# Kernel optimization log

Measured on AMD Instinct MI355X. Metric: run time of the kernel, lower is better.

The kernel has to match this reference:

```python
import jax, jax.numpy as jnp
import numpy as np

B, N, K, D, H = 4, 256, 32, 32, 8
NUM_SPATIAL, NUM_EDGES = 512, 1024


def setup_inputs() -> dict:
    key = jax.random.key(0)
    k1, k2, k3, k4, k5 = jax.random.split(key, 5)
    spatial_pos = jax.random.randint(k1, (B, N, N), 0, NUM_SPATIAL, dtype=jnp.int64)
    edge_input = jax.random.randint(k2, (B, N, N, K), 0, NUM_EDGES + 1, dtype=jnp.int64)
    spatial_emb = jax.random.normal(k3, (NUM_SPATIAL, H), dtype=jnp.float32)
    spatial_emb = spatial_emb.at[0].set(0.0)  # padding_idx=0
    edge_feat_emb = jax.random.normal(k4, (NUM_EDGES + 1, D), dtype=jnp.float32)
    edge_feat_emb = edge_feat_emb.at[0].set(0.0)  # padding_idx=0
    edge_pos_emb = jax.random.normal(k5, (K, D * H), dtype=jnp.float32)
    return {"spatial_pos": spatial_pos, "edge_input": edge_input,
            "spatial_emb": spatial_emb, "edge_feat_emb": edge_feat_emb,
            "edge_pos_emb": edge_pos_emb}


def reference(spatial_pos, edge_input, spatial_emb, edge_feat_emb, edge_pos_emb):
    # spatial bias: gather [B,N,N,H] -> [B,H,N,N]
    spatial_bias = jnp.transpose(spatial_emb[spatial_pos], (0, 3, 1, 2))
    # edge feature gather: [B,N,N,K,D]
    edge_feat = edge_feat_emb[edge_input]
    pos_weight = edge_pos_emb.reshape(K, D, H)  # [K,D,H]
    # per-hop projection then mean over valid hops
    terms = jnp.einsum('bnmkd,kdh->bnmkh', edge_feat, pos_weight)  # [B,N,N,K,H]
    mask = (edge_input != 0)
    path_len = jnp.maximum(mask.sum(axis=-1, keepdims=True).astype(terms.dtype), 1.0)  # [B,N,N,1]
    edge_bias = terms.sum(axis=-2) / path_len  # [B,N,N,H]
    edge_bias = jnp.transpose(edge_bias, (0, 3, 1, 2))  # [B,H,N,N]
    return spatial_bias + edge_bias
```

## Files before the change

kernel.cpp:

```cpp
#include <hip/hip_runtime.h>
#include <hip/hip_bf16.h>

#define BB 4
#define NN 256
#define KK 32
#define DD 32
#define HH 8
#define NROWS 1024
#define NPTS (BB * NN * NN)
#define NNSQ (NN * NN)
#define TPB 1024
#define NBLK (NPTS / TPB)
#define SLICE_US (NROWS * HH)
#define SLOT_US  (2 * SLICE_US)

typedef __attribute__((ext_vector_type(8))) unsigned short ushort8;
typedef __attribute__((ext_vector_type(4))) int iv4;

#define FENCE  asm volatile("" ::: "memory")
#define LGKM0  asm volatile("s_waitcnt lgkmcnt(0)" ::: "memory")
#define BAR    __builtin_amdgcn_s_barrier()
#define VMW(n) asm volatile("s_waitcnt vmcnt(" #n ")" ::: "memory")

__device__ __forceinline__ unsigned short f2bf(float f) {
    unsigned u = __float_as_uint(f);
    unsigned r = (u + 0x7FFFu + ((u >> 16) & 1u)) >> 16;
    return (unsigned short)r;
}

__device__ __forceinline__ void gload16(const void* g, void* l) {
    __builtin_amdgcn_global_load_lds(
        (const __attribute__((address_space(1))) void*)g,
        (__attribute__((address_space(3))) void*)l,
        16, 0, 0);
}

__global__ __launch_bounds__(256) void build_proj_bf16(
    const float* __restrict__ feat,
    const float* __restrict__ w,
    unsigned short* __restrict__ proj)
{
    int t  = blockIdx.x * 256 + threadIdx.x;
    int k  = t >> 10;
    int e  = (t & 1023) + 1;

    const float* frow = feat + (size_t)e * DD;
    const float* wrow = w + (size_t)k * DD * HH;

    float acc[HH];
#pragma unroll
    for (int h = 0; h < HH; ++h) acc[h] = 0.0f;

#pragma unroll
    for (int d = 0; d < DD; ++d) {
        float f = frow[d];
#pragma unroll
        for (int h = 0; h < HH; ++h) acc[h] = fmaf(f, wrow[d * HH + h], acc[h]);
    }

    ushort8 o;
#pragma unroll
    for (int h = 0; h < HH; ++h) o[h] = f2bf(acc[h]);
    *(ushort8*)(proj + (size_t)t * HH) = o;
}

template <int E>
__global__ __launch_bounds__(TPB) void attn_bias_v8(
    const int* __restrict__ sp,
    const int* __restrict__ ei,
    const float* __restrict__ semb,
    const unsigned short* __restrict__ proj,
    float* __restrict__ out)
{
    __shared__ __align__(16) unsigned short tbuf[3 * SLOT_US];
    __shared__ __align__(16) unsigned short zrow[8];
    __shared__ unsigned int ibuf[2][4][NROWS + 4];

    const int tid = threadIdx.x;
    const int p0  = blockIdx.x * TPB;
    const int pg  = p0 + tid;

    constexpr int NC = (E == 2) ? 4 : 2;
    const iv4* EI4 = (const iv4*)ei;
    const size_t bi4 = (size_t)p0 * (8 * E);

    iv4 cv[NC];

    auto issueC = [&](int g) {
#pragma unroll
        for (int c = 0; c < NC; ++c) {
            if (E == 2) {
                int j = c * TPB + tid, pt = j >> 2, q = j & 3;
                cv[c] = EI4[bi4 + (size_t)pt * 16 + 4 * g + q];
            } else {
                int j = c * TPB + tid, pt = j >> 1, q = j & 1;
                cv[c] = EI4[bi4 + (size_t)pt * 8 + 2 * g + q];
            }
        }
    };
    auto writeC = [&](int nb) {
#pragma unroll
        for (int c = 0; c < NC; ++c) {
            if (E == 2) {
                int j = c * TPB + tid, pt = j >> 2, q = j & 3;
                ibuf[nb][q][pt] = ((unsigned)cv[c].x & 0xffffu) |
                                  ((unsigned)cv[c].z << 16);
            } else {
                int j = c * TPB + tid, pt = j >> 1, q = j & 1;
                ibuf[nb][2 * q][pt] = ((unsigned)cv[c].x & 0xffffu) |
                                      ((unsigned)cv[c].y << 16);
                ibuf[nb][2 * q + 1][pt] = ((unsigned)cv[c].z & 0xffffu) |
                                          ((unsigned)cv[c].w << 16);
            }
        }
    };
    auto stage2 = [&](int phn, int slot) {
        gload16(proj + (size_t)(2 * phn) * SLICE_US + tid * HH,
                &tbuf[slot * SLOT_US + tid * HH]);
        gload16(proj + (size_t)(2 * phn + 1) * SLICE_US + tid * HH,
                &tbuf[slot * SLOT_US + SLICE_US + tid * HH]);
    };

    float acc[HH];
#pragma unroll
    for (int h = 0; h < HH; ++h) acc[h] = 0.0f;
    int cnt = 0;

    auto dohops = [&](int slot, int gsel, int q) {
        unsigned pr = ibuf[gsel][q][tid];
        int e0 = pr & 0xffffu;
        int e1 = pr >> 16;
        cnt += (e0 != 0) + (e1 != 0);
        const unsigned short* tb = &tbuf[slot * SLOT_US];
        const unsigned short* a0 = e0 ? tb + (e0 - 1) * HH : zrow;
        const unsigned short* a1 = e1 ? tb + SLICE_US + (e1 - 1) * HH : zrow;
        ushort8 w0 = *(const ushort8*)a0;
        ushort8 w1 = *(const ushort8*)a1;
#pragma unroll
        for (int h = 0; h < HH; ++h) {
            acc[h] += __uint_as_float(((unsigned)w0[h]) << 16);
            acc[h] += __uint_as_float(((unsigned)w1[h]) << 16);
        }
    };

#define VMWA do { if constexpr (E == 2) VMW(6); else VMW(4); } while (0)
#define ENDPH do { FENCE; VMW(2); LGKM0; BAR; } while (0)

    int sv = (E == 2) ? (int)((const long long*)sp)[pg] : sp[pg];
    FENCE;
    issueC(0);
    FENCE;
    stage2(0, 0);
    stage2(1, 1);
    if (tid == 0) *(float4*)zrow = make_float4(0.f, 0.f, 0.f, 0.f);
    FENCE;
    writeC(0);
    issueC(1);
    FENCE;
    VMWA; LGKM0; BAR;

    stage2(2, 2);  FENCE; dohops(0, 0, 0); FENCE; VMWA; LGKM0; BAR;
    stage2(3, 0);  FENCE; dohops(1, 0, 1); ENDPH;
    stage2(4, 1);  FENCE; dohops(2, 0, 2); ENDPH;
    stage2(5, 2);  FENCE; dohops(0, 0, 3); writeC(1); issueC(2);
                   FENCE; VMWA; LGKM0; BAR;
    stage2(6, 0);  FENCE; dohops(1, 1, 0); FENCE; VMWA; LGKM0; BAR;
    stage2(7, 1);  FENCE; dohops(2, 1, 1); ENDPH;
    stage2(8, 2);  FENCE; dohops(0, 1, 2); ENDPH;
    stage2(9, 0);  FENCE; dohops(1, 1, 3); writeC(0); issueC(3);
                   FENCE; VMWA; LGKM0; BAR;
    stage2(10, 1); FENCE; dohops(2, 0, 0); FENCE; VMWA; LGKM0; BAR;
    stage2(11, 2); FENCE; dohops(0, 0, 1); ENDPH;
    stage2(12, 0); FENCE; dohops(1, 0, 2); ENDPH;
    stage2(13, 1); FENCE; dohops(2, 0, 3); writeC(1); ENDPH;
    stage2(14, 2); FENCE; dohops(0, 1, 0); ENDPH;
    stage2(15, 0); FENCE; dohops(1, 1, 1); ENDPH;
    dohops(2, 1, 2); FENCE; VMW(0); LGKM0; BAR;
    dohops(0, 1, 3);

    const float4* srow = (const float4*)(semb + (size_t)sv * HH);
    float4 s0v = srow[0], s1v = srow[1];
    float sb[HH] = {s0v.x, s0v.y, s0v.z, s0v.w, s1v.x, s1v.y, s1v.z, s1v.w};

    float inv = 1.0f / (float)(cnt ? cnt : 1);
    float* o = out + (size_t)(pg >> 16) * (HH * NNSQ) + (pg & (NNSQ - 1));
#pragma unroll
    for (int h = 0; h < HH; ++h)
        o[(size_t)h * NNSQ] = sb[h] + acc[h] * inv;
}

extern "C" void kernel_launch(void* const* d_in, const int* in_sizes, int n_in,
                              void* d_out, int out_size, void* d_ws, size_t ws_size,
                              hipStream_t stream) {
    const int*   sp = (const int*)d_in[0];
    const int*   ei = (const int*)d_in[1];
    const float* se = (const float*)d_in[2];
    const float* fe = (const float*)d_in[3];
    const float* pw = (const float*)d_in[4];
    float* out = (float*)d_out;

    const bool i64 = (in_sizes[0] == 2 * NPTS);
    unsigned short* proj = (unsigned short*)d_ws;

    build_proj_bf16<<<128, 256, 0, stream>>>(fe, pw, proj);

    if (i64) attn_bias_v8<2><<<NBLK, TPB, 0, stream>>>(sp, ei, se, proj, out);
    else     attn_bias_v8<1><<<NBLK, TPB, 0, stream>>>(sp, ei, se, proj, out);
}
```

Measured before the change: 25.81 us.

## Precompact edge indices to 16-bit pairs in a fused pre-pass kernel

```diff
diff --git a/kernel.cpp b/kernel.cpp
--- a/kernel.cpp
+++ b/kernel.cpp
@@ -13,9 +13,14 @@
 #define NBLK (NPTS / TPB)
 #define SLICE_US (NROWS * HH)
 #define SLOT_US  (2 * SLICE_US)
+#define CMP_U32 (NPTS * 16)
+#define CMP_BYTES ((size_t)CMP_U32 * 4)
+#define PROJ_BYTES ((size_t)KK * NROWS * HH * 2)
+#define NEED_WS (CMP_BYTES + PROJ_BYTES)
 
 typedef __attribute__((ext_vector_type(8))) unsigned short ushort8;
 typedef __attribute__((ext_vector_type(4))) int iv4;
+typedef __attribute__((ext_vector_type(2))) int iv2;
 
 #define FENCE  asm volatile("" ::: "memory")
 #define LGKM0  asm volatile("s_waitcnt lgkmcnt(0)" ::: "memory")
@@ -35,45 +40,151 @@
         16, 0, 0);
 }
 
+__device__ __forceinline__ void build_one(int t, const float* __restrict__ feat,
+                                          const float* __restrict__ w,
+                                          unsigned short* __restrict__ proj) {
+    int k = t >> 10;
+    int e = (t & 1023) + 1;
+    const float* frow = feat + (size_t)e * DD;
+    const float* wrow = w + (size_t)k * DD * HH;
+    float acc[HH];
+#pragma unroll
+    for (int h = 0; h < HH; ++h) acc[h] = 0.0f;
+#pragma unroll
+    for (int d = 0; d < DD; ++d) {
+        float f = frow[d];
+#pragma unroll
+        for (int h = 0; h < HH; ++h) acc[h] = fmaf(f, wrow[d * HH + h], acc[h]);
+    }
+    ushort8 o;
+#pragma unroll
+    for (int h = 0; h < HH; ++h) o[h] = f2bf(acc[h]);
+    *(ushort8*)(proj + (size_t)t * HH) = o;
+}
+
 __global__ __launch_bounds__(256) void build_proj_bf16(
-    const float* __restrict__ feat,
-    const float* __restrict__ w,
+    const float* __restrict__ feat, const float* __restrict__ w,
+    unsigned short* __restrict__ proj) {
+    build_one(blockIdx.x * 256 + threadIdx.x, feat, w, proj);
+}
+
+template <int E>
+__global__ __launch_bounds__(256) void fused_pre(
+    const int* __restrict__ ei, const float* __restrict__ feat,
+    const float* __restrict__ w, unsigned* __restrict__ cmp,
     unsigned short* __restrict__ proj)
 {
-    int t  = blockIdx.x * 256 + threadIdx.x;
-    int k  = t >> 10;
-    int e  = (t & 1023) + 1;
-
-    const float* frow = feat + (size_t)e * DD;
-    const float* wrow = w + (size_t)k * DD * HH;
-
-    float acc[HH];
-#pragma unroll
-    for (int h = 0; h < HH; ++h) acc[h] = 0.0f;
-
-#pragma unroll
-    for (int d = 0; d < DD; ++d) {
-        float f = frow[d];
-#pragma unroll
-        for (int h = 0; h < HH; ++h) acc[h] = fmaf(f, wrow[d * HH + h], acc[h]);
+    int bid = blockIdx.x;
+    int tid = threadIdx.x;
+    if (bid < 128) { build_one(bid * 256 + tid, feat, w, proj); return; }
+
+    const iv4* EI4 = (const iv4*)ei;
+    size_t g = (size_t)(bid - 128) * 256 + tid;
+    if (E == 2) {
+        iv4 v = EI4[g];
+        cmp[g] = ((unsigned)v.x & 0xffffu) | ((unsigned)v.z << 16);
+    } else {
+        iv4 v = EI4[g];
+        iv2 o;
+        o.x = (int)(((unsigned)v.x & 0xffffu) | ((unsigned)v.y << 16));
+        o.y = (int)(((unsigned)v.z & 0xffffu) | ((unsigned)v.w << 16));
+        ((iv2*)cmp)[g] = o;
     }
-
-    ushort8 o;
-#pragma unroll
-    for (int h = 0; h < HH; ++h) o[h] = f2bf(acc[h]);
-    *(ushort8*)(proj + (size_t)t * HH) = o;
 }
 
 template <int E>
-__global__ __launch_bounds__(TPB) void attn_bias_v8(
+__global__ __launch_bounds__(TPB) void attn_bias_v14(
     const int* __restrict__ sp,
-    const int* __restrict__ ei,
+    const unsigned* __restrict__ cmp,
     const float* __restrict__ semb,
     const unsigned short* __restrict__ proj,
     float* __restrict__ out)
 {
     __shared__ __align__(16) unsigned short tbuf[3 * SLOT_US];
     __shared__ __align__(16) unsigned short zrow[8];
+
+    const int tid = threadIdx.x;
+    const int pg  = blockIdx.x * TPB + tid;
+
+    float acc[HH];
+#pragma unroll
+    for (int h = 0; h < HH; ++h) acc[h] = 0.0f;
+    int cnt = 0;
+
+#define K2STG(q) do{                                                           \
+        gload16(proj + (size_t)(2 * (q)) * SLICE_US + (size_t)tid * 8,         \
+                &tbuf[((q) % 3) * SLOT_US + tid * 8]);                         \
+        gload16(proj + (size_t)(2 * (q) + 1) * SLICE_US + (size_t)tid * 8,     \
+                &tbuf[((q) % 3) * SLOT_US + SLICE_US + tid * 8]);              \
+    }while(0)
+
+#define K2HOP(p, pr) do{                                                       \
+        unsigned _pr = (unsigned)(pr);                                         \
+        int e0 = _pr & 0xffffu;                                                \
+        int e1 = _pr >> 16;                                                    \
+        cnt += (e0 != 0) + (e1 != 0);                                          \
+        const unsigned short* tb = &tbuf[((p) % 3) * SLOT_US];                 \
+        const unsigned short* a0 = e0 ? tb + (e0 - 1) * HH : zrow;             \
+        const unsigned short* a1 = e1 ? tb + SLICE_US + (e1 - 1) * HH : zrow;  \
+        ushort8 w0 = *(const ushort8*)a0;                                      \
+        ushort8 w1 = *(const ushort8*)a1;                                      \
+        _Pragma("unroll")                                                      \
+        for (int h = 0; h < HH; ++h) {                                         \
+            acc[h] += __uint_as_float(((unsigned)w0[h]) << 16);                \
+            acc[h] += __uint_as_float(((unsigned)w1[h]) << 16);                \
+        }                                                                      \
+    }while(0)
+
+#define K2PH(p, pr) do{                                                        \
+        if ((p) <= 13) K2STG((p) + 2);                                         \
+        K2HOP(p, pr);                                                          \
+        FENCE; VMW(2); BAR;                                                    \
+    }while(0)
+
+    int sv;
+    if constexpr (E == 2) sv = (int)((const long long*)sp)[pg];
+    else                  sv = sp[pg];
+    FENCE;
+    const iv4* C4 = (const iv4*)cmp;
+    iv4 P0 = C4[(size_t)pg * 4 + 0];
+    iv4 P1 = C4[(size_t)pg * 4 + 1];
+    iv4 P2 = C4[(size_t)pg * 4 + 2];
+    iv4 P3 = C4[(size_t)pg * 4 + 3];
+    FENCE;
+    K2STG(0); K2STG(1);
+    if (tid == 0) *(float4*)zrow = make_float4(0.f, 0.f, 0.f, 0.f);
+    FENCE;
+    VMW(2);
+    LGKM0;
+    BAR;
+
+    K2PH(0,  P0.x); K2PH(1,  P0.y); K2PH(2,  P0.z); K2PH(3,  P0.w);
+    K2PH(4,  P1.x); K2PH(5,  P1.y); K2PH(6,  P1.z); K2PH(7,  P1.w);
+    K2PH(8,  P2.x); K2PH(9,  P2.y); K2PH(10, P2.z); K2PH(11, P2.w);
+    K2PH(12, P3.x);
+    K2PH(13, P3.y);
+    K2HOP(14, P3.z); FENCE; VMW(0); BAR;
+    K2HOP(15, P3.w);
+
+    const float4* srow = (const float4*)(semb + (size_t)sv * HH);
+    float4 s0v = srow[0], s1v = srow[1];
+    float sb[HH] = {s0v.x, s0v.y, s0v.z, s0v.w, s1v.x, s1v.y, s1v.z, s1v.w};
+
+    float inv = 1.0f / (float)(cnt ? cnt : 1);
+    float* o = out + (size_t)(pg >> 16) * (HH * NNSQ) + (pg & (NNSQ - 1));
+#pragma unroll
+    for (int h = 0; h < HH; ++h)
+        o[(size_t)h * NNSQ] = sb[h] + acc[h] * inv;
+}
+
+template <int E>
+__global__ __launch_bounds__(TPB) void attn_bias_v8(
+    const int* __restrict__ sp, const int* __restrict__ ei,
+    const float* __restrict__ semb, const unsigned short* __restrict__ proj,
+    float* __restrict__ out)
+{
+    __shared__ __align__(16) unsigned short tbuf[3 * SLOT_US];
+    __shared__ __align__(16) unsigned short zrow[8];
     __shared__ unsigned int ibuf[2][4][NROWS + 4];
 
     const int tid = threadIdx.x;
@@ -82,7 +193,7 @@
 
     constexpr int NC = (E == 2) ? 4 : 2;
     const iv4* EI4 = (const iv4*)ei;
-    const size_t bi4 = (size_t)p0 * (8 * E);
+    const size_t bi4 = (size_t)blockIdx.x * TPB * (8 * E);
 
     iv4 cv[NC];
 
@@ -200,10 +311,21 @@
     float* out = (float*)d_out;
 
     const bool i64 = (in_sizes[0] == 2 * NPTS);
-    unsigned short* proj = (unsigned short*)d_ws;
-
-    build_proj_bf16<<<128, 256, 0, stream>>>(fe, pw, proj);
-
-    if (i64) attn_bias_v8<2><<<NBLK, TPB, 0, stream>>>(sp, ei, se, proj, out);
-    else     attn_bias_v8<1><<<NBLK, TPB, 0, stream>>>(sp, ei, se, proj, out);
-}
+
+    if (ws_size >= NEED_WS) {
+        unsigned* cmp = (unsigned*)d_ws;
+        unsigned short* proj = (unsigned short*)((char*)d_ws + CMP_BYTES);
+        if (i64) {
+            fused_pre<2><<<128 + 16384, 256, 0, stream>>>(ei, fe, pw, cmp, proj);
+            attn_bias_v14<2><<<NBLK, TPB, 0, stream>>>(sp, cmp, se, proj, out);
+        } else {
+            fused_pre<1><<<128 + 8192, 256, 0, stream>>>(ei, fe, pw, cmp, proj);
+            attn_bias_v14<1><<<NBLK, TPB, 0, stream>>>(sp, cmp, se, proj, out);
+        }
+    } else {
+        unsigned short* proj = (unsigned short*)d_ws;
+        build_proj_bf16<<<128, 256, 0, stream>>>(fe, pw, proj);
+        if (i64) attn_bias_v8<2><<<NBLK, TPB, 0, stream>>>(sp, ei, se, proj, out);
+        else     attn_bias_v8<1><<<NBLK, TPB, 0, stream>>>(sp, ei, se, proj, out);
+    }
+}
```

After: 27.28 us. +5.7%, slower.
